# Kernel tuning notes

Hardware: AMD Instinct MI355X
Metric: run time of the kernel (lower is better)

Reference implementation:

```python
import jax, jax.numpy as jnp
import numpy as np

B, N, E1, H, D = 16, 256, 4, 8, 128  # batch, max nodes, edge types+1, heads, dim
VOCAB = 100


def setup_inputs() -> dict:
    key = jax.random.key(0)
    ks = jax.random.split(key, 20)
    s = 0.05
    return dict(
        node_feat=jax.random.randint(ks[0], (B, N), 0, VOCAB),
        L=jax.random.normal(ks[1], (B, N, N, E1), jnp.float32),
        emb=jax.random.normal(ks[2], (VOCAB, D), jnp.float32) * s,
        W0=jax.random.normal(ks[3], (E1, H, D, D), jnp.float32) * s,
        W1=jax.random.normal(ks[4], (E1, H, D * H * E1, D), jnp.float32) * (s / 4.0),
        a1w0=jax.random.normal(ks[5], (E1, H, D), jnp.float32) * s,
        a1b0=jnp.zeros((E1, H), jnp.float32),
        a2w0=jax.random.normal(ks[6], (E1, H, D), jnp.float32) * s,
        a2b0=jnp.zeros((E1, H), jnp.float32),
        a1w1=jax.random.normal(ks[7], (E1, H, D), jnp.float32) * s,
        a1b1=jnp.zeros((E1, H), jnp.float32),
        a2w1=jax.random.normal(ks[8], (E1, H, D), jnp.float32) * s,
        a2b1=jnp.zeros((E1, H), jnp.float32),
        sb0=jnp.zeros((E1, H, D), jnp.float32),
        sb1=jnp.zeros((E1, H, D), jnp.float32),
        outW=jax.random.normal(ks[9], (D, D), jnp.float32) * s,
        outb=jnp.zeros((D,), jnp.float32),
        attW=jax.random.normal(ks[10], (D,), jnp.float32) * s,
        attb=jnp.zeros((), jnp.float32),
    )


def _gat_layer(state, Ltr, W, a1w, a1b, a2w, a2b, sb, last):
    # state: (B, N, Din); W: (E1, H, Din, D); Ltr: (E1, 1, B, N, N)
    Wh = jnp.einsum('bni,ehio->ehbno', state, W)                      # (E1,H,B,N,D)
    s1 = jnp.einsum('ehbno,eho->ehbn', Wh, a1w) + a1b[:, :, None, None]
    s2 = jnp.einsum('ehbno,eho->ehbn', Wh, a2w) + a2b[:, :, None, None]
    logits = jax.nn.leaky_relu(s1[..., :, None] + s2[..., None, :], 0.2) + Ltr
    att = jax.nn.softmax(logits, axis=3)  # torch softmax over dim=1 of (B,N,N)
    h = jnp.einsum('ehbnm,ehbmo->ehbno', att, Wh) + sb[:, :, None, None, :]
    if last:
        return jnp.mean(h, axis=(0, 1))                               # (B,N,D)
    h = jax.nn.elu(h)
    # concat order in torch: outer edge-type jj, inner head ii -> (B,N,E1*H*D)
    return jnp.transpose(h, (2, 3, 0, 1, 4)).reshape(state.shape[0], state.shape[1], -1)


def reference(node_feat, L, emb, W0, W1, a1w0, a1b0, a2w0, a2b0,
              a1w1, a1b1, a2w1, a2b1, sb0, sb1, outW, outb, attW, attb):
    Ltr = jnp.transpose(L, (3, 0, 1, 2))[:, None]  # (E1,1,B,N,N)
    state = emb[node_feat]                         # (B,N,D)
    state = _gat_layer(state, Ltr, W0, a1w0, a1b0, a2w0, a2b0, sb0, last=False)
    state = _gat_layer(state, Ltr, W1, a1w1, a1b1, a2w1, a2b1, sb1, last=True)
    y = state @ outW + outb                        # (B,N,D)
    aw = jax.nn.sigmoid(state @ attW + attb)       # (B,N)
    y = aw[..., None] * y
    return jnp.mean(y, axis=1)                     # (B,D)
```

## Files before the change

### kernel.cpp

```cpp
#include <hip/hip_runtime.h>
#include <hip/hip_bf16.h>

#define Bq 16
#define Nq 256
#define E1q 4
#define Hq 8
#define Dq 128
#define EH 32
#define BN 4096

typedef __hip_bfloat16 bf16;
typedef short bf16x8 __attribute__((ext_vector_type(8)));
typedef float f32x4 __attribute__((ext_vector_type(4)));

__device__ __forceinline__ void gll16(const void* gptr, void* lptr) {
    __builtin_amdgcn_global_load_lds(
        (const __attribute__((address_space(1))) void*)gptr,
        (__attribute__((address_space(3))) void*)lptr, 16, 0, 0);
}

__device__ __forceinline__ unsigned short f2bf(float v) {
    __hip_bfloat16 h = __float2bfloat16(v);
    return *(unsigned short*)&h;
}

__device__ __forceinline__ void transpose_tile(const float* __restrict__ W,
                                               bf16* __restrict__ WT, int K,
                                               int kt, int nt, int eh,
                                               float (*tile)[65], int tid) {
    int tr = tid >> 6, tc = tid & 63;
    const float* src = W + ((size_t)eh * K + kt * 64) * 128 + nt * 64;
#pragma unroll
    for (int p = 0; p < 16; ++p) {
        int r = p * 4 + tr;
        tile[r][tc] = src[(size_t)r * 128 + tc];
    }
    __syncthreads();
    bf16* dst = WT + ((size_t)eh * 128 + nt * 64) * K + kt * 64;
#pragma unroll
    for (int p = 0; p < 16; ++p) {
        int n = p * 4 + tr;
        dst[(size_t)n * K + tc] = __float2bfloat16(tile[tc][n]);
    }
}

__global__ __launch_bounds__(256) void prep_kernel(const int* __restrict__ nf,
                                                   const float* __restrict__ emb,
                                                   const float* __restrict__ W0,
                                                   const float* __restrict__ W1,
                                                   const float* __restrict__ L,
                                                   bf16* __restrict__ st0b,
                                                   bf16* __restrict__ W0T,
                                                   bf16* __restrict__ W1T,
                                                   float* __restrict__ Le) {
    int bid = blockIdx.x;
    int t = threadIdx.x;
    __shared__ float tile[64][65];
    if (bid < 2048) {
        int i = bid * 256 + t;
        int row = i >> 7, col = i & 127;
        st0b[i] = __float2bfloat16(emb[nf[row] * Dq + col]);
    } else if (bid < 2176) {
        int id2 = bid - 2048;
        transpose_tile(W0, W0T, 128, id2 & 1, (id2 >> 1) & 1, id2 >> 2, tile, t);
    } else if (bid < 6272) {
        int id3 = bid - 2176;
        transpose_tile(W1, W1T, 4096, id3 & 63, (id3 >> 6) & 1, id3 >> 7, tile, t);
    } else {
        int idx = (bid - 6272) * 256 + t;
        float4 v = *(const float4*)(L + (size_t)idx * 4);
        Le[idx] = v.x;
        Le[1048576 + idx] = v.y;
        Le[2097152 + idx] = v.z;
        Le[3145728 + idx] = v.w;
    }
}

__global__ __launch_bounds__(256) void mfma_gemm_kernel(const bf16* __restrict__ Ab,
                                                        const bf16* __restrict__ Bt,
                                                        bf16* __restrict__ Wht,
                                                        const float* __restrict__ a1w,
                                                        const float* __restrict__ a1b,
                                                        const float* __restrict__ a2w,
                                                        const float* __restrict__ a2b,
                                                        float* __restrict__ s1,
                                                        float* __restrict__ s2, int K) {
    int id = blockIdx.x;
    int xcd = id & 7, slot = id >> 3;
    int eh = (slot & 3) * 8 + xcd;
    int rt = slot >> 2;
    int tid = threadIdx.x;
    int w = tid >> 6, l = tid & 63;
    int q = l >> 4, mn = l & 15;
    __shared__ __align__(16) bf16 As[128 * 64];
    __shared__ __align__(16) bf16 Bs[128 * 64];
    __shared__ float red1[128], red2[128];
    const bf16* Ap = Ab + (size_t)(rt * 128) * K;
    const bf16* Bp = Bt + (size_t)eh * 128 * K;
    int lr = l >> 3;
    int g = (l & 7) ^ lr;
    int gcol = g * 8;

    if (tid < 128) { red1[tid] = 0.f; red2[tid] = 0.f; }

    f32x4 acc[4][4];
#pragma unroll
    for (int i = 0; i < 4; i++)
#pragma unroll
        for (int j = 0; j < 4; j++) acc[i][j] = (f32x4){0.f, 0.f, 0.f, 0.f};

    int wr = (w >> 1) * 64, wc = (w & 1) * 64;
    int msw = mn & 7;

    for (int k0 = 0; k0 < K; k0 += 64) {
#pragma unroll
        for (int u = 0; u < 4; ++u) {
            int i = w * 4 + u;
            int r = i * 8 + lr;
            gll16(Ap + (size_t)r * K + k0 + gcol, (char*)As + i * 1024);
            gll16(Bp + (size_t)r * K + k0 + gcol, (char*)Bs + i * 1024);
        }
        __syncthreads();
#pragma unroll
        for (int kk = 0; kk < 2; ++kk) {
            int qb = ((kk * 4 + q) ^ msw) * 16;
            bf16x8 af[4], bfr[4];
#pragma unroll
            for (int i = 0; i < 4; ++i) {
                af[i]  = *(const bf16x8*)((const char*)As + (wr + i * 16 + mn) * 128 + qb);
                bfr[i] = *(const bf16x8*)((const char*)Bs + (wc + i * 16 + mn) * 128 + qb);
            }
#pragma unroll
            for (int i = 0; i < 4; ++i)
#pragma unroll
                for (int j = 0; j < 4; ++j)
                    acc[i][j] = __builtin_amdgcn_mfma_f32_16x16x32_bf16(af[i], bfr[j], acc[i][j], 0, 0, 0);
        }
        __syncthreads();
    }
#pragma unroll
    for (int i = 0; i < 4; ++i) {
        int r0 = rt * 128 + wr + i * 16 + q * 4;
        int b = r0 >> 8, m = r0 & 255;
#pragma unroll
        for (int j = 0; j < 4; ++j) {
            int o = wc + j * 16 + mn;
            ushort4 pk;
            pk.x = f2bf(acc[i][j][0]);
            pk.y = f2bf(acc[i][j][1]);
            pk.z = f2bf(acc[i][j][2]);
            pk.w = f2bf(acc[i][j][3]);
            *(ushort4*)(Wht + ((((size_t)eh * 16 + b) * 128 + o) * 256 + m)) = pk;
        }
    }
    float w1v[4], w2v[4];
#pragma unroll
    for (int j = 0; j < 4; ++j) {
        int o = wc + j * 16 + mn;
        w1v[j] = a1w[eh * 128 + o];
        w2v[j] = a2w[eh * 128 + o];
    }
#pragma unroll
    for (int i = 0; i < 4; ++i)
#pragma unroll
        for (int r = 0; r < 4; ++r) {
            float p1 = 0.f, p2 = 0.f;
#pragma unroll
            for (int j = 0; j < 4; ++j) {
                p1 += acc[i][j][r] * w1v[j];
                p2 += acc[i][j][r] * w2v[j];
            }
#pragma unroll
            for (int off = 1; off < 16; off <<= 1) {
                p1 += __shfl_xor(p1, off);
                p2 += __shfl_xor(p2, off);
            }
            if (mn == 0) {
                int row = wr + i * 16 + q * 4 + r;
                atomicAdd(&red1[row], p1);
                atomicAdd(&red2[row], p2);
            }
        }
    __syncthreads();
    if (tid < 128) {
        int rg = rt * 128 + tid;
        s1[eh * 4096 + rg] = red1[tid] + a1b[eh];
        s2[eh * 4096 + rg] = red2[tid] + a2b[eh];
    }
}

__global__ __launch_bounds__(512, 2) void gemm4k_kernel(const bf16* __restrict__ Ab,
                                                        const bf16* __restrict__ Bt,
                                                        bf16* __restrict__ Wht,
                                                        const float* __restrict__ a1w,
                                                        const float* __restrict__ a1b,
                                                        const float* __restrict__ a2w,
                                                        const float* __restrict__ a2b,
                                                        float* __restrict__ s1,
                                                        float* __restrict__ s2) {
    __shared__ __align__(16) char smem[131072];
    int bid = blockIdx.x;
    int wg = (bid & 7) * 32 + (bid >> 3);
    int tm = wg >> 4, tn = wg & 15;
    int tid = threadIdx.x;
    int wid = tid >> 6, l = tid & 63;
    int wr = wid >> 2, wc = wid & 3;
    int lhi = l >> 4, llo = l & 15;
    int sa = (lhi ^ ((l >> 1) & 3)) << 4;
    int skq = (l & 3) ^ ((l >> 3) & 3);

    const bf16* Ap = Ab + (size_t)tm * 256 * 4096;
    const bf16* Bp = Bt + (size_t)tn * 256 * 4096;
    const bf16* sA = Ap + (size_t)(wid * 16 + (l >> 2)) * 4096 + skq * 8;
    const bf16* sB = Bp + (size_t)(wid * 16 + (l >> 2)) * 4096 + skq * 8;
    char* dA = (char*)smem + wid * 1024;
    char* dB = (char*)smem + 65536 + wid * 1024;

    auto stageA = [&](int tt) {
        int bo = (tt & 3) * 16384;
        gll16(sA + tt * 32, dA + bo);
        gll16(sA + (size_t)128 * 4096 + tt * 32, dA + bo + 8192);
    };
    auto stageB = [&](int tt) {
        int bo = (tt & 3) * 16384;
        gll16(sB + tt * 32, dB + bo);
        gll16(sB + (size_t)128 * 4096 + tt * 32, dB + bo + 8192);
    };

    f32x4 acc[8][4];
#pragma unroll
    for (int i = 0; i < 8; ++i)
#pragma unroll
        for (int j = 0; j < 4; ++j) acc[i][j] = (f32x4){0.f, 0.f, 0.f, 0.f};

    int aoff = ((wr * 64 + llo) << 6) + sa;
    int boff[4];
#pragma unroll
    for (int n = 0; n < 4; ++n)
        boff[n] = 65536 + (((n >> 1) * 128 + wc * 32 + (n & 1) * 16 + llo) << 6) + sa;

    stageA(0); stageB(0); stageA(1); stageB(1); stageA(2); stageB(2);
    asm volatile("s_waitcnt vmcnt(8)" ::: "memory");
    __builtin_amdgcn_s_barrier();

#pragma unroll 1
    for (int t = 0; t < 128; ++t) {
        int bo = (t & 3) * 16384;
        const char* sm = (const char*)smem;
        bf16x8 af[4], bv[4];
#pragma unroll
        for (int m = 0; m < 4; ++m)
            af[m] = *(const bf16x8*)(sm + bo + aoff + m * 1024);
#pragma unroll
        for (int n = 0; n < 4; ++n)
            bv[n] = *(const bf16x8*)(sm + bo + boff[n]);
        if (t < 125) stageA(t + 3);
        __builtin_amdgcn_s_barrier();
        asm volatile("s_waitcnt lgkmcnt(0)" ::: "memory");
        __builtin_amdgcn_sched_barrier(0);
        __builtin_amdgcn_s_setprio(1);
#pragma unroll
        for (int m = 0; m < 4; ++m)
#pragma unroll
            for (int n = 0; n < 4; ++n)
                acc[m][n] = __builtin_amdgcn_mfma_f32_16x16x32_bf16(af[m], bv[n], acc[m][n], 0, 0, 0);
        __builtin_amdgcn_s_setprio(0);
        __builtin_amdgcn_s_barrier();
#pragma unroll
        for (int m = 0; m < 4; ++m)
            af[m] = *(const bf16x8*)(sm + bo + aoff + 8192 + m * 1024);
        if (t < 125) {
            stageB(t + 3);
            asm volatile("s_waitcnt vmcnt(8)" ::: "memory");
        } else if (t == 125) {
            asm volatile("s_waitcnt vmcnt(4)" ::: "memory");
        } else if (t == 126) {
            asm volatile("s_waitcnt vmcnt(0)" ::: "memory");
        }
        __builtin_amdgcn_s_barrier();
        asm volatile("s_waitcnt lgkmcnt(0)" ::: "memory");
        __builtin_amdgcn_sched_barrier(0);
        __builtin_amdgcn_s_setprio(1);
#pragma unroll
        for (int m = 0; m < 4; ++m)
#pragma unroll
            for (int n = 0; n < 4; ++n)
                acc[4 + m][n] = __builtin_amdgcn_mfma_f32_16x16x32_bf16(af[m], bv[n], acc[4 + m][n], 0, 0, 0);
        __builtin_amdgcn_s_setprio(0);
        __builtin_amdgcn_s_barrier();
    }

    float* red = (float*)smem;
    red[tid] = 0.f;
    red[tid + 512] = 0.f;
    float w1v[4], w2v[4];
#pragma unroll
    for (int n = 0; n < 4; ++n) {
        int eh = tn * 2 + (n >> 1);
        int o = wc * 32 + (n & 1) * 16 + llo;
        w1v[n] = a1w[eh * 128 + o];
        w2v[n] = a2w[eh * 128 + o];
    }
    __syncthreads();
#pragma unroll
    for (int mi = 0; mi < 8; ++mi) {
        int R = (mi >> 2) * 128 + wr * 64 + (mi & 3) * 16 + lhi * 4;
#pragma unroll
        for (int n = 0; n < 4; ++n) {
            int eh = tn * 2 + (n >> 1);
            int o = wc * 32 + (n & 1) * 16 + llo;
            ushort4 pk;
            pk.x = f2bf(acc[mi][n][0]);
            pk.y = f2bf(acc[mi][n][1]);
            pk.z = f2bf(acc[mi][n][2]);
            pk.w = f2bf(acc[mi][n][3]);
            *(ushort4*)(Wht + ((((size_t)eh * 16 + tm) * 128 + o) * 256 + R)) = pk;
        }
#pragma unroll
        for (int r = 0; r < 4; ++r) {
            float p10 = acc[mi][0][r] * w1v[0] + acc[mi][1][r] * w1v[1];
            float p11 = acc[mi][2][r] * w1v[2] + acc[mi][3][r] * w1v[3];
            float p20 = acc[mi][0][r] * w2v[0] + acc[mi][1][r] * w2v[1];
            float p21 = acc[mi][2][r] * w2v[2] + acc[mi][3][r] * w2v[3];
#pragma unroll
            for (int off = 1; off < 16; off <<= 1) {
                p10 += __shfl_xor(p10, off);
                p11 += __shfl_xor(p11, off);
                p20 += __shfl_xor(p20, off);
                p21 += __shfl_xor(p21, off);
            }
            if (llo == 0) {
                int row = R + r;
                atomicAdd(&red[row], p10);
                atomicAdd(&red[256 + row], p11);
                atomicAdd(&red[512 + row], p20);
                atomicAdd(&red[768 + row], p21);
            }
        }
    }
    __syncthreads();
    {
        int ehl = tid >> 8, row = tid & 255;
        int eh = tn * 2 + ehl;
        s1[eh * 4096 + tm * 256 + row] = red[ehl * 256 + row] + a1b[eh];
        s2[eh * 4096 + tm * 256 + row] = red[512 + ehl * 256 + row] + a2b[eh];
    }
}

__global__ __launch_bounds__(256) void colsoft_kernel(const float* __restrict__ s1,
                                                      const float* __restrict__ s2,
                                                      const float* __restrict__ Le,
                                                      float4* __restrict__ stat) {
    int mt = blockIdx.x, b = blockIdx.y, e = blockIdx.z;
    int t = threadIdx.x;
    __shared__ float Lt[256 * 32];
    __shared__ float s1L[8 * 256];
#pragma unroll
    for (int i = 0; i < 8; ++i) s1L[i * 256 + t] = s1[(e * 8 + i) * 4096 + b * 256 + t];
    const float* Lb = Le + ((size_t)(e * 16 + b) * 256) * 256 + mt * 32;
#pragma unroll
    for (int j = 0; j < 8; ++j) {
        int f = t + 256 * j;
        int n = f >> 3, c4 = (f & 7) * 4;
        *(float4*)(Lt + n * 32 + c4) = *(const float4*)(Lb + (size_t)n * 256 + c4);
    }
    __syncthreads();
    int h = t >> 5, mm = t & 31;
    int m = mt * 32 + mm;
    float s2v = s2[(e * 8 + h) * 4096 + b * 256 + m];
    const float* s1p = s1L + h * 256;
    float s1max = -1e30f;
#pragma unroll
    for (int u = 0; u < 8; ++u) s1max = fmaxf(s1max, s1p[mm * 8 + u]);
#pragma unroll
    for (int off = 16; off; off >>= 1) s1max = fmaxf(s1max, __shfl_xor(s1max, off));
    float sm = s1max + s2v;
    float bound = (sm > 0.f ? sm : 0.2f * sm) + 8.0f;
    float sum = 0.f;
    for (int n = 0; n < 256; ++n) {
        float x = s1p[n] + s2v;
        x = x > 0.f ? x : 0.2f * x;
        x += Lt[n * 32 + mm];
        sum += __expf(x - bound);
    }
    float4 st = {s2v, bound, 1.0f / sum, 0.f};
    stat[(e * 8 + h) * 4096 + b * 256 + m] = st;
}

template <int LAST>
__global__ __launch_bounds__(256) void att_mfma_kernel(const float* __restrict__ s1,
                                                       const float4* __restrict__ stat,
                                                       const float* __restrict__ Le,
                                                       const bf16* __restrict__ Wht,
                                                       const float* __restrict__ sb,
                                                       bf16* __restrict__ outb) {
    int nt = blockIdx.x;
    int b = blockIdx.y;
    int eh = blockIdx.z;
    int e = eh >> 3;
    int tid = threadIdx.x;
    int w = tid >> 6, l = tid & 63;
    int q = l >> 4, mn = l & 15;
    __shared__ __align__(16) bf16 As[128 * 32];
    __shared__ __align__(16) bf16 Bs[128 * 40];
    __shared__ float s1L[128];
    __shared__ __align__(16) float4 stL[256];

    int base = eh * 4096 + b * 256;
    if (tid < 128) s1L[tid] = s1[base + nt * 128 + tid];
    stL[tid] = stat[base + tid];
    __syncthreads();

    const bf16* Whtp = Wht + ((size_t)eh * 16 + b) * 32768;
    int nl = tid >> 1, mh = (tid & 1) * 16;
    const float* Lrow = Le + (((size_t)(e * 16 + b) * 256) + nt * 128 + nl) * 256;
    float s1v = s1L[nl];
    int srow = l >> 2;
    int sq = (l & 3) ^ ((l >> 3) & 3);
    int scol = sq * 8;
    int rsw = ((mn >> 1) & 3) << 3;

    f32x4 acc[4][4];
#pragma unroll
    for (int i = 0; i < 4; i++)
#pragma unroll
        for (int j = 0; j < 4; j++) acc[i][j] = (f32x4){0.f, 0.f, 0.f, 0.f};

    int wr = (w >> 1) * 64, wc = (w & 1) * 64;

    float4 lv[4];
#pragma unroll
    for (int jj = 0; jj < 4; ++jj) lv[jj] = *(const float4*)(Lrow + mh + jj * 4);

    for (int k0 = 0; k0 < 256; k0 += 32) {
#pragma unroll
        for (int u = 0; u < 2; ++u) {
            int i = 2 * w + u;
            gll16(Whtp + (size_t)(i * 16 + srow) * 256 + k0 + scol, (char*)As + i * 1024);
        }
        float4 cur[4];
#pragma unroll
        for (int jj = 0; jj < 4; ++jj) cur[jj] = lv[jj];
        if (k0 + 32 < 256) {
#pragma unroll
            for (int jj = 0; jj < 4; ++jj)
                lv[jj] = *(const float4*)(Lrow + k0 + 32 + mh + jj * 4);
        }
#pragma unroll
        for (int jj = 0; jj < 4; ++jj) {
            int mb = mh + jj * 4;
            float av[4];
#pragma unroll
            for (int c = 0; c < 4; ++c) {
                int m = k0 + mb + c;
                float4 stv = stL[m];
                float x = s1v + stv.x;
                x = x > 0.f ? x : 0.2f * x;
                x += ((const float*)&cur[jj])[c];
                av[c] = __expf(x - stv.y) * stv.z;
            }
            unsigned int u01 = (unsigned int)f2bf(av[0]) | ((unsigned int)f2bf(av[1]) << 16);
            unsigned int u23 = (unsigned int)f2bf(av[2]) | ((unsigned int)f2bf(av[3]) << 16);
            unsigned int* bp = (unsigned int*)Bs + (nl * 40 + mb) / 2;
            bp[0] = u01;
            bp[1] = u23;
        }
        __syncthreads();
        bf16x8 af[4], bfr[4];
#pragma unroll
        for (int i = 0; i < 4; ++i) {
            af[i]  = *(const bf16x8*)(As + (wr + i * 16 + mn) * 32 + ((q << 3) ^ rsw));
            bfr[i] = *(const bf16x8*)(Bs + (wc + i * 16 + mn) * 40 + q * 8);
        }
#pragma unroll
        for (int i = 0; i < 4; ++i)
#pragma unroll
            for (int j = 0; j < 4; ++j)
                acc[i][j] = __builtin_amdgcn_mfma_f32_16x16x32_bf16(af[i], bfr[j], acc[i][j], 0, 0, 0);
        __syncthreads();
    }
#pragma unroll
    for (int i = 0; i < 4; ++i) {
        int o0 = wr + i * 16 + q * 4;
        float4 sbv = *(const float4*)(sb + eh * 128 + o0);
#pragma unroll
        for (int j = 0; j < 4; ++j) {
            int n = wc + j * 16 + mn;
            float v0 = acc[i][j][0] + sbv.x;
            float v1 = acc[i][j][1] + sbv.y;
            float v2 = acc[i][j][2] + sbv.z;
            float v3 = acc[i][j][3] + sbv.w;
            if (LAST == 0) {
                v0 = v0 > 0.f ? v0 : __expf(v0) - 1.f;
                v1 = v1 > 0.f ? v1 : __expf(v1) - 1.f;
                v2 = v2 > 0.f ? v2 : __expf(v2) - 1.f;
                v3 = v3 > 0.f ? v3 : __expf(v3) - 1.f;
                ushort4 pk = {f2bf(v0), f2bf(v1), f2bf(v2), f2bf(v3)};
                *(ushort4*)(outb + (size_t)(b * 256 + nt * 128 + n) * 4096 + eh * Dq + o0) = pk;
            } else {
                ushort4 pk = {f2bf(v0), f2bf(v1), f2bf(v2), f2bf(v3)};
                *(ushort4*)(outb + ((size_t)eh * 4096 + b * 256 + nt * 128 + n) * Dq + o0) = pk;
            }
        }
    }
}

__global__ __launch_bounds__(256) void reduce_aw_kernel(const bf16* __restrict__ h2b,
                                                        const float* __restrict__ attW,
                                                        const float* __restrict__ attb,
                                                        float* __restrict__ st2,
                                                        float* __restrict__ aw) {
    int t = threadIdx.x;
    int rl = t >> 7, o = t & 127;
    int r = blockIdx.x * 2 + rl;
    float acc = 0.f;
#pragma unroll
    for (int eh = 0; eh < EH; ++eh)
        acc += __bfloat162float(h2b[((size_t)eh * 4096 + r) * 128 + o]);
    acc *= (1.0f / 32.0f);
    st2[(size_t)r * 128 + o] = acc;
    float p = acc * attW[o];
#pragma unroll
    for (int off = 32; off; off >>= 1) p += __shfl_down(p, off);
    __shared__ float part[4];
    if ((t & 63) == 0) part[t >> 6] = p;
    __syncthreads();
    if (t == 0) aw[r] = 1.0f / (1.0f + __expf(-(part[0] + part[1] + attb[0])));
    if (t == 128) aw[r] = 1.0f / (1.0f + __expf(-(part[2] + part[3] + attb[0])));
}

__global__ __launch_bounds__(128) void final_kernel(const float* __restrict__ st2,
                                                    const float* __restrict__ aw,
                                                    const float* __restrict__ outW,
                                                    const float* __restrict__ outb,
                                                    float* __restrict__ out) {
    int b = blockIdx.x;
    int t = threadIdx.x;
    __shared__ float awL[256], zL[128];
    awL[t] = aw[b * 256 + t];
    awL[t + 128] = aw[b * 256 + t + 128];
    __syncthreads();
    float z = 0.f;
    for (int n = 0; n < 256; ++n) z += awL[n] * st2[(size_t)(b * 256 + n) * Dq + t];
    float sa = 0.f;
    for (int n = 0; n < 256; ++n) sa += awL[n];
    zL[t] = z;
    __syncthreads();
    float acc = sa * outb[t];
    for (int o = 0; o < Dq; ++o) acc += zL[o] * outW[o * Dq + t];
    out[b * Dq + t] = acc * (1.0f / 256.0f);
}

extern "C" void kernel_launch(void* const* d_in, const int* in_sizes, int n_in,
                              void* d_out, int out_size, void* d_ws, size_t ws_size,
                              hipStream_t stream) {
    const int* nf = (const int*)d_in[0];
    const float* L = (const float*)d_in[1];
    const float* emb = (const float*)d_in[2];
    const float* W0 = (const float*)d_in[3];
    const float* W1 = (const float*)d_in[4];
    const float* a1w0 = (const float*)d_in[5];
    const float* a1b0 = (const float*)d_in[6];
    const float* a2w0 = (const float*)d_in[7];
    const float* a2b0 = (const float*)d_in[8];
    const float* a1w1 = (const float*)d_in[9];
    const float* a1b1 = (const float*)d_in[10];
    const float* a2w1 = (const float*)d_in[11];
    const float* a2b1 = (const float*)d_in[12];
    const float* sb0 = (const float*)d_in[13];
    const float* sb1 = (const float*)d_in[14];
    const float* outW = (const float*)d_in[15];
    const float* outb = (const float*)d_in[16];
    const float* attW = (const float*)d_in[17];
    const float* attb = (const float*)d_in[18];

    char* p = (char*)d_ws;
    bf16* st0b = (bf16*)(p);
    bf16* W0T  = (bf16*)(p + 1048576);
    bf16* W1T  = (bf16*)(p + 2097152);
    bf16* st1b = (bf16*)(p + 35651584);
    bf16* h2b  = (bf16*)(p + 2097152);
    float* Le  = (float*)(p + 69206016);
    bf16* Wht  = (bf16*)(p + 85983232);
    float* s1  = (float*)(p + 119537664);
    float* s2  = (float*)(p + 120061952);
    float4* stat = (float4*)(p + 120586240);
    float* st2 = (float*)(p);
    float* aw  = s1;
    float* outp = (float*)d_out;

    prep_kernel<<<10368, 256, 0, stream>>>(nf, emb, W0, W1, L, st0b, W0T, W1T, Le);

    mfma_gemm_kernel<<<1024, 256, 0, stream>>>(st0b, W0T, Wht, a1w0, a1b0, a2w0, a2b0, s1, s2, 128);
    colsoft_kernel<<<dim3(8, 16, 4), 256, 0, stream>>>(s1, s2, Le, stat);
    att_mfma_kernel<0><<<dim3(2, 16, 32), 256, 0, stream>>>(s1, stat, Le, Wht, sb0, st1b);

    gemm4k_kernel<<<256, 512, 0, stream>>>(st1b, W1T, Wht, a1w1, a1b1, a2w1, a2b1, s1, s2);
    colsoft_kernel<<<dim3(8, 16, 4), 256, 0, stream>>>(s1, s2, Le, stat);
    att_mfma_kernel<1><<<dim3(2, 16, 32), 256, 0, stream>>>(s1, stat, Le, Wht, sb1, h2b);

    reduce_aw_kernel<<<2048, 256, 0, stream>>>(h2b, attW, attb, st2, aw);
    final_kernel<<<16, 128, 0, stream>>>(st2, aw, outW, outb, outp);
}
```

Measured before the change: 421.6 us.

## Issue all LDS fragment loads upfront and cut per-iteration barriers in GEMM loop

Result: no change. 422.6 us (+0.2%).

```diff
diff --git a/kernel.cpp b/kernel.cpp
--- a/kernel.cpp
+++ b/kernel.cpp
@@ -247,46 +247,51 @@
     for (int t = 0; t < 128; ++t) {
         int bo = (t & 3) * 16384;
         const char* sm = (const char*)smem;
-        bf16x8 af[4], bv[4];
-#pragma unroll
-        for (int m = 0; m < 4; ++m)
-            af[m] = *(const bf16x8*)(sm + bo + aoff + m * 1024);
+        bf16x8 a0[4], a1[4], bb[4];
+        bb[0] = *(const bf16x8*)(sm + bo + boff[0]);
+        bb[1] = *(const bf16x8*)(sm + bo + boff[1]);
+        bb[2] = *(const bf16x8*)(sm + bo + boff[2]);
+        bb[3] = *(const bf16x8*)(sm + bo + boff[3]);
+        a0[0] = *(const bf16x8*)(sm + bo + aoff);
+        __builtin_amdgcn_sched_barrier(0);
+        a0[1] = *(const bf16x8*)(sm + bo + aoff + 1024);
+        a0[2] = *(const bf16x8*)(sm + bo + aoff + 2048);
+        a0[3] = *(const bf16x8*)(sm + bo + aoff + 3072);
+        __builtin_amdgcn_sched_barrier(0);
+        a1[0] = *(const bf16x8*)(sm + bo + aoff + 8192);
+        a1[1] = *(const bf16x8*)(sm + bo + aoff + 8192 + 1024);
+        a1[2] = *(const bf16x8*)(sm + bo + aoff + 8192 + 2048);
+        a1[3] = *(const bf16x8*)(sm + bo + aoff + 8192 + 3072);
+        __builtin_amdgcn_sched_barrier(0);
+        if (t < 125) { stageA(t + 3); stageB(t + 3); }
+        asm volatile("s_waitcnt lgkmcnt(7)" ::: "memory");
+        __builtin_amdgcn_sched_barrier(0);
+        __builtin_amdgcn_s_setprio(1);
 #pragma unroll
         for (int n = 0; n < 4; ++n)
-            bv[n] = *(const bf16x8*)(sm + bo + boff[n]);
-        if (t < 125) stageA(t + 3);
-        __builtin_amdgcn_s_barrier();
+            acc[0][n] = __builtin_amdgcn_mfma_f32_16x16x32_bf16(a0[0], bb[n], acc[0][n], 0, 0, 0);
+        asm volatile("s_waitcnt lgkmcnt(4)" ::: "memory");
+        __builtin_amdgcn_sched_barrier(0);
+#pragma unroll
+        for (int m = 1; m < 4; ++m)
+#pragma unroll
+            for (int n = 0; n < 4; ++n)
+                acc[m][n] = __builtin_amdgcn_mfma_f32_16x16x32_bf16(a0[m], bb[n], acc[m][n], 0, 0, 0);
         asm volatile("s_waitcnt lgkmcnt(0)" ::: "memory");
         __builtin_amdgcn_sched_barrier(0);
-        __builtin_amdgcn_s_setprio(1);
 #pragma unroll
         for (int m = 0; m < 4; ++m)
 #pragma unroll
             for (int n = 0; n < 4; ++n)
-                acc[m][n] = __builtin_amdgcn_mfma_f32_16x16x32_bf16(af[m], bv[n], acc[m][n], 0, 0, 0);
+                acc[4 + m][n] = __builtin_amdgcn_mfma_f32_16x16x32_bf16(a1[m], bb[n], acc[4 + m][n], 0, 0, 0);
         __builtin_amdgcn_s_setprio(0);
-        __builtin_amdgcn_s_barrier();
-#pragma unroll
-        for (int m = 0; m < 4; ++m)
-            af[m] = *(const bf16x8*)(sm + bo + aoff + 8192 + m * 1024);
         if (t < 125) {
-            stageB(t + 3);
             asm volatile("s_waitcnt vmcnt(8)" ::: "memory");
         } else if (t == 125) {
             asm volatile("s_waitcnt vmcnt(4)" ::: "memory");
         } else if (t == 126) {
             asm volatile("s_waitcnt vmcnt(0)" ::: "memory");
         }
-        __builtin_amdgcn_s_barrier();
-        asm volatile("s_waitcnt lgkmcnt(0)" ::: "memory");
-        __builtin_amdgcn_sched_barrier(0);
-        __builtin_amdgcn_s_setprio(1);
-#pragma unroll
-        for (int m = 0; m < 4; ++m)
-#pragma unroll
-            for (int n = 0; n < 4; ++n)
-                acc[4 + m][n] = __builtin_amdgcn_mfma_f32_16x16x32_bf16(af[m], bv[n], acc[4 + m][n], 0, 0, 0);
-        __builtin_amdgcn_s_setprio(0);
         __builtin_amdgcn_s_barrier();
     }
 
```

## Register double-buffer LDS fragments and collapse GEMM loop to one barrier

Applied to the files above, without the earlier changes.

Result: slower. 441.2 us (+4.6%).

```diff
diff --git a/kernel.cpp b/kernel.cpp
--- a/kernel.cpp
+++ b/kernel.cpp
@@ -240,54 +240,56 @@
         boff[n] = 65536 + (((n >> 1) * 128 + wc * 32 + (n & 1) * 16 + llo) << 6) + sa;
 
     stageA(0); stageB(0); stageA(1); stageB(1); stageA(2); stageB(2);
-    asm volatile("s_waitcnt vmcnt(8)" ::: "memory");
+    asm volatile("s_waitcnt vmcnt(4)" ::: "memory");
     __builtin_amdgcn_s_barrier();
+    const char* sm = (const char*)smem;
+    bf16x8 cb[4], ca0[4], ca1[4];
+#pragma unroll
+    for (int n = 0; n < 4; ++n) cb[n] = *(const bf16x8*)(sm + boff[n]);
+#pragma unroll
+    for (int m = 0; m < 4; ++m) ca0[m] = *(const bf16x8*)(sm + aoff + m * 1024);
+#pragma unroll
+    for (int m = 0; m < 4; ++m) ca1[m] = *(const bf16x8*)(sm + aoff + 8192 + m * 1024);
 
 #pragma unroll 1
     for (int t = 0; t < 128; ++t) {
-        int bo = (t & 3) * 16384;
-        const char* sm = (const char*)smem;
-        bf16x8 af[4], bv[4];
-#pragma unroll
-        for (int m = 0; m < 4; ++m)
-            af[m] = *(const bf16x8*)(sm + bo + aoff + m * 1024);
-#pragma unroll
-        for (int n = 0; n < 4; ++n)
-            bv[n] = *(const bf16x8*)(sm + bo + boff[n]);
-        if (t < 125) stageA(t + 3);
-        __builtin_amdgcn_s_barrier();
-        asm volatile("s_waitcnt lgkmcnt(0)" ::: "memory");
+        int bo1 = ((t + 1) & 3) * 16384;
+        bf16x8 nb[4], na0[4], na1[4];
+        if (t < 127) {
+#pragma unroll
+            for (int n = 0; n < 4; ++n) nb[n] = *(const bf16x8*)(sm + bo1 + boff[n]);
+#pragma unroll
+            for (int m = 0; m < 4; ++m) na0[m] = *(const bf16x8*)(sm + bo1 + aoff + m * 1024);
+        }
+        if (t < 125) { stageA(t + 3); stageB(t + 3); }
+        if (t < 127) { asm volatile("s_waitcnt lgkmcnt(8)" ::: "memory"); }
+        else         { asm volatile("s_waitcnt lgkmcnt(0)" ::: "memory"); }
         __builtin_amdgcn_sched_barrier(0);
         __builtin_amdgcn_s_setprio(1);
 #pragma unroll
         for (int m = 0; m < 4; ++m)
 #pragma unroll
             for (int n = 0; n < 4; ++n)
-                acc[m][n] = __builtin_amdgcn_mfma_f32_16x16x32_bf16(af[m], bv[n], acc[m][n], 0, 0, 0);
+                acc[m][n] = __builtin_amdgcn_mfma_f32_16x16x32_bf16(ca0[m], cb[n], acc[m][n], 0, 0, 0);
+        if (t < 127) {
+#pragma unroll
+            for (int m = 0; m < 4; ++m) na1[m] = *(const bf16x8*)(sm + bo1 + aoff + 8192 + m * 1024);
+        }
+#pragma unroll
+        for (int m = 0; m < 4; ++m)
+#pragma unroll
+            for (int n = 0; n < 4; ++n)
+                acc[4 + m][n] = __builtin_amdgcn_mfma_f32_16x16x32_bf16(ca1[m], cb[n], acc[4 + m][n], 0, 0, 0);
         __builtin_amdgcn_s_setprio(0);
+        if (t < 125)       { asm volatile("s_waitcnt vmcnt(4)" ::: "memory"); }
+        else if (t == 125) { asm volatile("s_waitcnt vmcnt(0)" ::: "memory"); }
         __builtin_amdgcn_s_barrier();
-#pragma unroll
-        for (int m = 0; m < 4; ++m)
-            af[m] = *(const bf16x8*)(sm + bo + aoff + 8192 + m * 1024);
-        if (t < 125) {
-            stageB(t + 3);
-            asm volatile("s_waitcnt vmcnt(8)" ::: "memory");
-        } else if (t == 125) {
-            asm volatile("s_waitcnt vmcnt(4)" ::: "memory");
-        } else if (t == 126) {
-            asm volatile("s_waitcnt vmcnt(0)" ::: "memory");
-        }
-        __builtin_amdgcn_s_barrier();
-        asm volatile("s_waitcnt lgkmcnt(0)" ::: "memory");
-        __builtin_amdgcn_sched_barrier(0);
-        __builtin_amdgcn_s_setprio(1);
-#pragma unroll
-        for (int m = 0; m < 4; ++m)
-#pragma unroll
-            for (int n = 0; n < 4; ++n)
-                acc[4 + m][n] = __builtin_amdgcn_mfma_f32_16x16x32_bf16(af[m], bv[n], acc[4 + m][n], 0, 0, 0);
-        __builtin_amdgcn_s_setprio(0);
-        __builtin_amdgcn_s_barrier();
+        if (t < 127) {
+#pragma unroll
+            for (int n = 0; n < 4; ++n) cb[n] = nb[n];
+#pragma unroll
+            for (int m = 0; m < 4; ++m) { ca0[m] = na0[m]; ca1[m] = na1[m]; }
+        }
     }
 
     float* red = (float*)smem;
```

## Restructure 4K GEMM mainloop to BK=64 double-buffer with quadrant ping-pong

Applied to the files above, without the earlier changes.

Result: no change. 424.0 us (+0.6%).

```diff
diff --git a/kernel.cpp b/kernel.cpp
--- a/kernel.cpp
+++ b/kernel.cpp
@@ -206,25 +206,20 @@
     int wid = tid >> 6, l = tid & 63;
     int wr = wid >> 2, wc = wid & 3;
     int lhi = l >> 4, llo = l & 15;
-    int sa = (lhi ^ ((l >> 1) & 3)) << 4;
-    int skq = (l & 3) ^ ((l >> 3) & 3);
+    int skq = (l & 7) ^ ((l >> 3) & 7);
 
     const bf16* Ap = Ab + (size_t)tm * 256 * 4096;
     const bf16* Bp = Bt + (size_t)tn * 256 * 4096;
-    const bf16* sA = Ap + (size_t)(wid * 16 + (l >> 2)) * 4096 + skq * 8;
-    const bf16* sB = Bp + (size_t)(wid * 16 + (l >> 2)) * 4096 + skq * 8;
+    const bf16* sA = Ap + (size_t)(wid * 8 + (l >> 3)) * 4096 + skq * 8;
+    const bf16* sB = Bp + (size_t)(wid * 8 + (l >> 3)) * 4096 + skq * 8;
     char* dA = (char*)smem + wid * 1024;
-    char* dB = (char*)smem + 65536 + wid * 1024;
-
-    auto stageA = [&](int tt) {
-        int bo = (tt & 3) * 16384;
-        gll16(sA + tt * 32, dA + bo);
-        gll16(sA + (size_t)128 * 4096 + tt * 32, dA + bo + 8192);
+    char* dB = (char*)smem + 32768 + wid * 1024;
+
+    auto stA = [&](int tt, int s) {
+        gll16(sA + (size_t)s * 64 * 4096 + tt * 64, dA + (tt & 1) * 65536 + s * 8192);
     };
-    auto stageB = [&](int tt) {
-        int bo = (tt & 3) * 16384;
-        gll16(sB + tt * 32, dB + bo);
-        gll16(sB + (size_t)128 * 4096 + tt * 32, dB + bo + 8192);
+    auto stB = [&](int tt, int s) {
+        gll16(sB + (size_t)s * 64 * 4096 + tt * 64, dB + (tt & 1) * 65536 + s * 8192);
     };
 
     f32x4 acc[8][4];
@@ -233,60 +228,98 @@
 #pragma unroll
         for (int j = 0; j < 4; ++j) acc[i][j] = (f32x4){0.f, 0.f, 0.f, 0.f};
 
-    int aoff = ((wr * 64 + llo) << 6) + sa;
-    int boff[4];
-#pragma unroll
-    for (int n = 0; n < 4; ++n)
-        boff[n] = 65536 + (((n >> 1) * 128 + wc * 32 + (n & 1) * 16 + llo) << 6) + sa;
-
-    stageA(0); stageB(0); stageA(1); stageB(1); stageA(2); stageB(2);
-    asm volatile("s_waitcnt vmcnt(8)" ::: "memory");
+    int kp0 = ((lhi)     ^ (llo & 7)) << 4;
+    int kp1 = ((4 + lhi) ^ (llo & 7)) << 4;
+    int aoff = (wr * 64 + llo) << 7;
+    int boff = 32768 + ((wc * 32 + llo) << 7);
+
+    stA(0, 0); stA(0, 1); stB(0, 0); stB(0, 1);
+    stA(0, 2); stA(0, 3); stB(0, 2); stB(0, 3);
+    asm volatile("s_waitcnt vmcnt(4)" ::: "memory");
     __builtin_amdgcn_s_barrier();
 
 #pragma unroll 1
-    for (int t = 0; t < 128; ++t) {
-        int bo = (t & 3) * 16384;
-        const char* sm = (const char*)smem;
-        bf16x8 af[4], bv[4];
-#pragma unroll
-        for (int m = 0; m < 4; ++m)
-            af[m] = *(const bf16x8*)(sm + bo + aoff + m * 1024);
-#pragma unroll
-        for (int n = 0; n < 4; ++n)
-            bv[n] = *(const bf16x8*)(sm + bo + boff[n]);
-        if (t < 125) stageA(t + 3);
+    for (int t = 0; t < 64; ++t) {
+        const char* sm = (const char*)smem + (t & 1) * 65536;
+        bf16x8 A0[4][2], A1[4][2], B0[2][2], B1[2][2];
+#pragma unroll
+        for (int m = 0; m < 4; ++m) {
+            A0[m][0] = *(const bf16x8*)(sm + aoff + m * 2048 + kp0);
+            A0[m][1] = *(const bf16x8*)(sm + aoff + m * 2048 + kp1);
+        }
+#pragma unroll
+        for (int n = 0; n < 2; ++n) {
+            B0[n][0] = *(const bf16x8*)(sm + boff + n * 2048 + kp0);
+            B0[n][1] = *(const bf16x8*)(sm + boff + n * 2048 + kp1);
+        }
+        if (t < 63) { stA(t + 1, 0); stA(t + 1, 1); }
+        asm volatile("s_waitcnt lgkmcnt(8)" ::: "memory");
         __builtin_amdgcn_s_barrier();
         asm volatile("s_waitcnt lgkmcnt(0)" ::: "memory");
         __builtin_amdgcn_sched_barrier(0);
         __builtin_amdgcn_s_setprio(1);
 #pragma unroll
-        for (int m = 0; m < 4; ++m)
-#pragma unroll
-            for (int n = 0; n < 4; ++n)
-                acc[m][n] = __builtin_amdgcn_mfma_f32_16x16x32_bf16(af[m], bv[n], acc[m][n], 0, 0, 0);
+        for (int ks = 0; ks < 2; ++ks)
+#pragma unroll
+            for (int m = 0; m < 4; ++m)
+#pragma unroll
+                for (int n = 0; n < 2; ++n)
+                    acc[m][n] = __builtin_amdgcn_mfma_f32_16x16x32_bf16(A0[m][ks], B0[n][ks], acc[m][n], 0, 0, 0);
         __builtin_amdgcn_s_setprio(0);
+        if (t < 63) { asm volatile("s_waitcnt vmcnt(4)" ::: "memory"); }
+        else        { asm volatile("s_waitcnt vmcnt(2)" ::: "memory"); }
         __builtin_amdgcn_s_barrier();
 #pragma unroll
-        for (int m = 0; m < 4; ++m)
-            af[m] = *(const bf16x8*)(sm + bo + aoff + 8192 + m * 1024);
-        if (t < 125) {
-            stageB(t + 3);
-            asm volatile("s_waitcnt vmcnt(8)" ::: "memory");
-        } else if (t == 125) {
-            asm volatile("s_waitcnt vmcnt(4)" ::: "memory");
-        } else if (t == 126) {
-            asm volatile("s_waitcnt vmcnt(0)" ::: "memory");
-        }
+        for (int m = 0; m < 4; ++m) {
+            A1[m][0] = *(const bf16x8*)(sm + aoff + 16384 + m * 2048 + kp0);
+            A1[m][1] = *(const bf16x8*)(sm + aoff + 16384 + m * 2048 + kp1);
+        }
+        if (t < 63) { stB(t + 1, 0); stB(t + 1, 1); }
         __builtin_amdgcn_s_barrier();
         asm volatile("s_waitcnt lgkmcnt(0)" ::: "memory");
         __builtin_amdgcn_sched_barrier(0);
         __builtin_amdgcn_s_setprio(1);
 #pragma unroll
-        for (int m = 0; m < 4; ++m)
-#pragma unroll
-            for (int n = 0; n < 4; ++n)
-                acc[4 + m][n] = __builtin_amdgcn_mfma_f32_16x16x32_bf16(af[m], bv[n], acc[4 + m][n], 0, 0, 0);
+        for (int ks = 0; ks < 2; ++ks)
+#pragma unroll
+            for (int m = 0; m < 4; ++m)
+#pragma unroll
+                for (int n = 0; n < 2; ++n)
+                    acc[4 + m][n] = __builtin_amdgcn_mfma_f32_16x16x32_bf16(A1[m][ks], B0[n][ks], acc[4 + m][n], 0, 0, 0);
         __builtin_amdgcn_s_setprio(0);
+        if (t < 63) { asm volatile("s_waitcnt vmcnt(4)" ::: "memory"); }
+        else        { asm volatile("s_waitcnt vmcnt(0)" ::: "memory"); }
+        __builtin_amdgcn_s_barrier();
+#pragma unroll
+        for (int n = 0; n < 2; ++n) {
+            B1[n][0] = *(const bf16x8*)(sm + boff + 16384 + n * 2048 + kp0);
+            B1[n][1] = *(const bf16x8*)(sm + boff + 16384 + n * 2048 + kp1);
+        }
+        if (t < 63) { stA(t + 1, 2); stA(t + 1, 3); }
+        __builtin_amdgcn_s_barrier();
+        asm volatile("s_waitcnt lgkmcnt(0)" ::: "memory");
+        __builtin_amdgcn_sched_barrier(0);
+        __builtin_amdgcn_s_setprio(1);
+#pragma unroll
+        for (int ks = 0; ks < 2; ++ks)
+#pragma unroll
+            for (int m = 0; m < 4; ++m)
+#pragma unroll
+                for (int n = 0; n < 2; ++n)
+                    acc[m][2 + n] = __builtin_amdgcn_mfma_f32_16x16x32_bf16(A0[m][ks], B1[n][ks], acc[m][2 + n], 0, 0, 0);
+        __builtin_amdgcn_s_setprio(0);
+        __builtin_amdgcn_s_barrier();
+        if (t < 63) { stB(t + 1, 2); stB(t + 1, 3); }
+        __builtin_amdgcn_s_setprio(1);
+#pragma unroll
+        for (int ks = 0; ks < 2; ++ks)
+#pragma unroll
+            for (int m = 0; m < 4; ++m)
+#pragma unroll
+                for (int n = 0; n < 2; ++n)
+                    acc[4 + m][2 + n] = __builtin_amdgcn_mfma_f32_16x16x32_bf16(A1[m][ks], B1[n][ks], acc[4 + m][2 + n], 0, 0, 0);
+        __builtin_amdgcn_s_setprio(0);
+        if (t < 63) { asm volatile("s_waitcnt vmcnt(4)" ::: "memory"); }
         __builtin_amdgcn_s_barrier();
     }
 
```
